# Kernel tuning notes

Measured on AMD Instinct MI355X. Metric: run time of the kernel, lower is better.

The kernel has to match this reference:

```python
import jax, jax.numpy as jnp
import numpy as np

N = 50000      # nodes
E = 1_000_000  # edges
EMB = 64       # out_channels per head
H = 2          # heads
HC = H * EMB   # 128 = concat output dim
HID = 128      # fc hidden size
NEG_SLOPE = 0.2


def _p(k, shape):
    return jax.random.normal(k, shape, dtype=jnp.float32) * 0.1


def setup_inputs() -> dict:
    key = jax.random.key(0)
    ks = jax.random.split(key, 24)
    inp = {
        "x": jax.random.normal(ks[0], (N, 1), dtype=jnp.float32),
        "edge_index": jax.random.randint(ks[1], (2, E), 0, N, dtype=jnp.int32),
        "edge_attr": jax.random.normal(ks[2], (E, 1), dtype=jnp.float32),
        "target_node_idx": 123,
        # conv1: GATv2Conv(1 -> 64, heads=2, edge_dim=1)
        "Wl1": _p(ks[3], (1, HC)), "bl1": jnp.zeros((HC,), jnp.float32),
        "Wr1": _p(ks[4], (1, HC)), "br1": jnp.zeros((HC,), jnp.float32),
        "We1": _p(ks[5], (1, HC)),
        "att1": _p(ks[6], (H, EMB)),
        "b1": jnp.zeros((HC,), jnp.float32),
        # conv2: GATv2Conv(128 -> 64, heads=2, edge_dim=1)
        "Wl2": _p(ks[7], (HC, HC)), "bl2": jnp.zeros((HC,), jnp.float32),
        "Wr2": _p(ks[8], (HC, HC)), "br2": jnp.zeros((HC,), jnp.float32),
        "We2": _p(ks[9], (1, HC)),
        "att2": _p(ks[10], (H, EMB)),
        "b2": jnp.zeros((HC,), jnp.float32),
        # fc: Linear(128 -> 128)
        "Wfc": _p(ks[11], (HC, HID)), "bfc": jnp.zeros((HID,), jnp.float32),
    }
    return inp


def add_self_loops(src, dst, edge_attr, n):
    loop = jnp.arange(n, dtype=src.dtype)
    fill = jnp.mean(edge_attr, axis=0)  # PyG fill_value='mean'
    src2 = jnp.concatenate([src, loop])
    dst2 = jnp.concatenate([dst, loop])
    ea2 = jnp.concatenate([edge_attr, jnp.broadcast_to(fill, (n, edge_attr.shape[1]))])
    return src2, dst2, ea2


def gatv2(x, src, dst, edge_attr, Wl, bl, Wr, br, We, att, bias, n):
    # x: [n, F_in]; per-head transforms -> [n, H, EMB]
    xl = (x @ Wl + bl).reshape(n, H, EMB)   # source transform
    xr = (x @ Wr + br).reshape(n, H, EMB)   # target transform
    ef = (edge_attr @ We).reshape(-1, H, EMB)
    # GATv2 attention: a^T LeakyReLU(xl_j + xr_i + e_ij)
    z = jax.nn.leaky_relu(xl[src] + xr[dst] + ef, NEG_SLOPE)  # [E', H, EMB]
    logits = jnp.einsum('ehc,hc->eh', z, att)                 # [E', H]
    # segment softmax over incoming edges per destination node
    m = jax.ops.segment_max(logits, dst, num_segments=n)[dst]
    ex = jnp.exp(logits - m)
    s = jax.ops.segment_sum(ex, dst, num_segments=n)[dst]
    alpha = ex / s                                            # [E', H]
    msg = xl[src] * alpha[:, :, None]                         # [E', H, EMB]
    out = jax.ops.segment_sum(msg, dst, num_segments=n)       # [n, H, EMB]
    return out.reshape(n, HC) + bias


def reference(x, edge_index, edge_attr, target_node_idx,
              Wl1, bl1, Wr1, br1, We1, att1, b1,
              Wl2, bl2, Wr2, br2, We2, att2, b2,
              Wfc, bfc):
    n = x.shape[0]
    src, dst, ea = add_self_loops(edge_index[0], edge_index[1], edge_attr, n)
    h = gatv2(x, src, dst, ea, Wl1, bl1, Wr1, br1, We1, att1, b1, n)
    h = jax.nn.relu(h)
    h = gatv2(h, src, dst, ea, Wl2, bl2, Wr2, br2, We2, att2, b2, n)
    target_emb = h[target_node_idx]          # [HC]
    return target_emb @ Wfc + bfc            # [HID]
```

## Files before the change

### kernel.cpp

```cpp
#include <hip/hip_runtime.h>
#include <hip/hip_bf16.h>

#define NEG_SLOPE 0.2f
#define THR    256
#define NB1    512
#define NB2    512
#define B1CAP  16
#define B2CAP  32
#define CAP1   512
#define CAPS   64
#define MAXDEG 256
#define NTAIL  (CAPS + 1)

#define OFF_PARTS  8
#define OFF_B1CNT  (OFF_PARTS + NB1)
#define OFF_B1SRC  (OFF_B1CNT + NB1)
#define OFF_B1EA   (OFF_B1SRC + NB1 * B1CAP)
#define OFF_B2CNT  (OFF_B1EA + NB1 * B1CAP)
#define OFF_B2SRC  (OFF_B2CNT + NB2)
#define OFF_B2DST  (OFF_B2SRC + NB2 * B2CAP)
#define OFF_B2EA   (OFF_B2DST + NB2 * B2CAP)
#define OFF_L1SRC  (OFF_B2EA + NB2 * B2CAP)
#define OFF_L1EA   (OFF_L1SRC + CAP1)
#define OFF_SLIST  (OFF_L1EA + CAP1)
#define OFF_XL2    (OFF_SLIST + CAPS)
#define OFF_XR2    (OFF_XL2 + CAPS * 128)

__device__ __forceinline__ float us2f(unsigned short s) {
    union { unsigned int u; float f; } c;
    c.u = ((unsigned int)s) << 16;
    return c.f;
}
template<bool F32>
__device__ __forceinline__ float tld(const void* p, int i) {
    if (F32) return ((const float*)p)[i];
    return us2f(((const unsigned short*)p)[i]);
}
__device__ __forceinline__ float ald_f(const float* p) {
    return __hip_atomic_load(p, __ATOMIC_RELAXED, __HIP_MEMORY_SCOPE_AGENT);
}

template<bool F32>
__device__ void scan1_body(const int* __restrict__ src, const int* __restrict__ dst,
                           const void* __restrict__ ea, int t, int E,
                           int* __restrict__ W) {
    __shared__ float sRed[4];
    __shared__ int   sCnt;
    __shared__ int   sIb[B1CAP];
    __shared__ float sFb[B1CAP];
    const int tid = threadIdx.x, bid = blockIdx.x;
    const int gid = bid * THR + tid, gs = NB1 * THR;
    const int E4 = E >> 2, rem = E & 3;
    float* parts = (float*)(W + OFF_PARTS);
    int*   b1cnt = W + OFF_B1CNT;
    int*   b1src = W + OFF_B1SRC;
    float* b1ea  = (float*)(W + OFF_B1EA);

    if (tid == 0) sCnt = 0;
    __syncthreads();
    float sum = 0.f;
    for (int j = gid; j < E4; j += gs) {
        int4 d4 = ((const int4*)dst)[j];
        float v0, v1, v2, v3;
        if (F32) {
            float4 e4 = ((const float4*)ea)[j];
            v0 = e4.x; v1 = e4.y; v2 = e4.z; v3 = e4.w;
        } else {
            ushort4 u4 = ((const ushort4*)ea)[j];
            v0 = us2f(u4.x); v1 = us2f(u4.y); v2 = us2f(u4.z); v3 = us2f(u4.w);
        }
        sum += (v0 + v1) + (v2 + v3);
        int base = 4 * j;
        if (d4.x == t) { int p = atomicAdd(&sCnt, 1); if (p < B1CAP) { sIb[p] = src[base+0]; sFb[p] = v0; } }
        if (d4.y == t) { int p = atomicAdd(&sCnt, 1); if (p < B1CAP) { sIb[p] = src[base+1]; sFb[p] = v1; } }
        if (d4.z == t) { int p = atomicAdd(&sCnt, 1); if (p < B1CAP) { sIb[p] = src[base+2]; sFb[p] = v2; } }
        if (d4.w == t) { int p = atomicAdd(&sCnt, 1); if (p < B1CAP) { sIb[p] = src[base+3]; sFb[p] = v3; } }
    }
    if (gid < rem) {
        int i = E4 * 4 + gid;
        float v = tld<F32>(ea, i);
        sum += v;
        if (dst[i] == t) { int p = atomicAdd(&sCnt, 1); if (p < B1CAP) { sIb[p] = src[i]; sFb[p] = v; } }
    }
    for (int o = 32; o > 0; o >>= 1) sum += __shfl_down(sum, o);
    if ((tid & 63) == 0) sRed[tid >> 6] = sum;
    __syncthreads();
    if (tid == 0) parts[bid] = sRed[0] + sRed[1] + sRed[2] + sRed[3];
    int bc = sCnt < B1CAP ? sCnt : B1CAP;
    if (tid == 0) b1cnt[bid] = bc;
    if (tid < bc) { b1src[bid * B1CAP + tid] = sIb[tid]; b1ea[bid * B1CAP + tid] = sFb[tid]; }
}

__global__ void __launch_bounds__(THR)
k_scan1(const void* __restrict__ x, const int* __restrict__ src,
        const int* __restrict__ dst, const void* __restrict__ ea,
        const int* __restrict__ tgt, int E, int* __restrict__ W) {
    __shared__ int sWeird;
    if (threadIdx.x == 0) sWeird = 0;
    __syncthreads();
    {
        const unsigned short* u = (const unsigned short*)x;
        int c = 0;
        for (int i = threadIdx.x; i < 2048; i += THR) {
            int e2 = (u[i] >> 7) & 0xFF;
            if (e2 == 0 || e2 >= 0xC0) c++;
        }
        for (int o = 32; o > 0; o >>= 1) c += __shfl_down(c, o);
        if ((threadIdx.x & 63) == 0) atomicAdd(&sWeird, c);
    }
    __syncthreads();
    bool f32 = sWeird >= 64;
    if (blockIdx.x == 0 && threadIdx.x == 0) W[3] = f32 ? 1 : 0;
    int t = tgt[0];
    if (f32) scan1_body<true >(src, dst, ea, t, E, W);
    else     scan1_body<false>(src, dst, ea, t, E, W);
}

template<bool F32>
__device__ void scan2_body(const int* __restrict__ src, const int* __restrict__ dst,
                           const void* __restrict__ ea, int tgt0, int E,
                           int* __restrict__ W) {
    __shared__ int   sS[CAPS];
    __shared__ int   sNs, sCnt;
    __shared__ int   sIb[B2CAP], sIb2[B2CAP];
    __shared__ float sFb[B2CAP];
    __shared__ int   sPfx[THR];
    __shared__ float sRed[4];
    const int tid = threadIdx.x, bid = blockIdx.x;
    const int gid = bid * THR + tid, gs = NB2 * THR;
    const int E4 = E >> 2, rem = E & 3;
    float* parts = (float*)(W + OFF_PARTS);
    int*   b1cnt = W + OFF_B1CNT;
    int*   b1src = W + OFF_B1SRC;
    float* b1ea  = (float*)(W + OFF_B1EA);
    int*   b2cnt = W + OFF_B2CNT;
    int*   b2src = W + OFF_B2SRC;
    int*   b2dst = W + OFF_B2DST;
    float* b2ea  = (float*)(W + OFF_B2EA);
    int*   l1src = W + OFF_L1SRC;
    float* l1ea  = (float*)(W + OFF_L1EA);
    int*   slist = W + OFF_SLIST;

    if (tid == 0) { sS[0] = tgt0; sNs = 1; sCnt = 0; }
    __syncthreads();
    for (int bk = tid; bk < NB1; bk += THR) {
        int c = b1cnt[bk]; if (c > B1CAP) c = B1CAP;
        for (int j = 0; j < c; j++) {
            int p = atomicAdd(&sNs, 1);
            if (p < CAPS) sS[p] = b1src[bk * B1CAP + j];
        }
    }
    __syncthreads();
    int ns = sNs < CAPS ? sNs : CAPS;

    #define CHECK(dv, idx)                                                     \
        do {                                                                   \
            for (int j_ = 0; j_ < ns; j_++) {                                  \
                if (sS[j_] == (dv)) {                                          \
                    int p_ = atomicAdd(&sCnt, 1);                              \
                    if (p_ < B2CAP) {                                          \
                        sIb[p_] = src[idx]; sIb2[p_] = (dv);                   \
                        sFb[p_] = tld<F32>(ea, idx);                           \
                    }                                                          \
                    break;                                                     \
                }                                                              \
            }                                                                  \
        } while (0)
    for (int j = gid; j < E4; j += gs) {
        int4 d4 = ((const int4*)dst)[j];
        int base = 4 * j;
        CHECK(d4.x, base + 0);
        CHECK(d4.y, base + 1);
        CHECK(d4.z, base + 2);
        CHECK(d4.w, base + 3);
    }
    if (gid < rem) { int i = E4 * 4 + gid; CHECK(dst[i], i); }
    #undef CHECK
    __syncthreads();
    int bc = sCnt < B2CAP ? sCnt : B2CAP;
    if (tid == 0) b2cnt[bid] = bc;
    if (tid < bc) {
        b2src[bid * B2CAP + tid] = sIb[tid];
        b2dst[bid * B2CAP + tid] = sIb2[tid];
        b2ea [bid * B2CAP + tid] = sFb[tid];
    }

    if (bid == 0) {
        __syncthreads();
        int c0  = b1cnt[2*tid];    if (c0  > B1CAP) c0  = B1CAP;
        int c1b = b1cnt[2*tid+1];  if (c1b > B1CAP) c1b = B1CAP;
        int c = c0 + c1b;
        sPfx[tid] = c;
        __syncthreads();
        for (int o = 1; o < THR; o <<= 1) {
            int v = (tid >= o) ? sPfx[tid - o] : 0;
            __syncthreads();
            sPfx[tid] += v;
            __syncthreads();
        }
        int base = sPfx[tid] - c;
        int c1tot = sPfx[THR - 1];
        for (int j = 0; j < c0; j++) {
            int p = base + j;
            if (p < CAP1 - 1) { l1src[p] = b1src[2*tid*B1CAP + j]; l1ea[p] = b1ea[2*tid*B1CAP + j]; }
        }
        for (int j = 0; j < c1b; j++) {
            int p = base + c0 + j;
            if (p < CAP1 - 1) { l1src[p] = b1src[(2*tid+1)*B1CAP + j]; l1ea[p] = b1ea[(2*tid+1)*B1CAP + j]; }
        }
        float s = parts[tid] + parts[tid + THR];
        for (int o = 32; o > 0; o >>= 1) s += __shfl_down(s, o);
        if ((tid & 63) == 0) sRed[tid >> 6] = s;
        __syncthreads();
        if (tid == 0) {
            float mean = (sRed[0] + sRed[1] + sRed[2] + sRed[3]) / (float)E;
            int c1 = c1tot < CAP1 - 1 ? c1tot : CAP1 - 1;
            l1src[c1] = tgt0; l1ea[c1] = mean;
            c1++;
            int nsl = 0;
            for (int e = 0; e < c1; e++) {
                int sv = l1src[e];
                bool f = false;
                for (int j = 0; j < nsl; j++) if (sS[j] == sv) { f = true; break; }
                if (!f && nsl < CAPS) { sS[nsl] = sv; nsl++; }
            }
            for (int j = 0; j < nsl; j++) slist[j] = sS[j];
            W[0] = c1; W[1] = nsl; W[4] = 0;
            ((float*)W)[5] = mean;
        }
    }
}

__global__ void __launch_bounds__(THR)
k_scan2(const int* __restrict__ src, const int* __restrict__ dst,
        const void* __restrict__ ea, const int* __restrict__ tgt,
        int E, int* __restrict__ W) {
    int t = tgt[0];
    if (W[3]) scan2_body<true >(src, dst, ea, t, E, W);
    else      scan2_body<false>(src, dst, ea, t, E, W);
}

template<bool F32>
__device__ void tail_body(
    const void* __restrict__ x, int tgt0,
    const void* Wl1, const void* bl1, const void* Wr1, const void* br1,
    const void* We1, const void* att1, const void* b1,
    const void* Wl2, const void* bl2, const void* Wr2, const void* br2,
    const void* We2, const void* att2, const void* b2v,
    const void* Wfc, const void* bfc,
    void* __restrict__ out, int* __restrict__ W)
{
    const int tid = threadIdx.x, bid = blockIdx.x;
    int*   b2cnt = W + OFF_B2CNT;
    int*   b2src = W + OFF_B2SRC;
    int*   b2dst = W + OFF_B2DST;
    float* b2ea  = (float*)(W + OFF_B2EA);
    int*   l1src = W + OFF_L1SRC;
    float* l1ea  = (float*)(W + OFF_L1EA);
    int*   slist = W + OFF_SLIST;
    float* xl2   = (float*)(W + OFF_XL2);
    float* xr2   = (float*)(W + OFF_XR2);

    int ns = W[1]; if (ns > CAPS) ns = CAPS;
    int c1 = W[0]; if (c1 > CAP1) c1 = CAP1;
    float mean = ((float*)W)[5];

    if (bid < ns) {
        __shared__ float sWl[128], sBl[128], sWe[128], sAtt[128], sB1[128], sBase[128];
        __shared__ float sXs[MAXDEG], sEa2[MAXDEG], sL0[MAXDEG], sL1[MAXDEG], sH[128];
        __shared__ int sCnt;
        int s = slist[bid];
        if (tid < 128) {
            sWl[tid] = tld<F32>(Wl1, tid);  sBl[tid] = tld<F32>(bl1, tid);
            sWe[tid] = tld<F32>(We1, tid);  sAtt[tid] = tld<F32>(att1, tid);
            sB1[tid] = tld<F32>(b1, tid);
            float xt = tld<F32>(x, s);
            sBase[tid] = xt * tld<F32>(Wr1, tid) + tld<F32>(br1, tid);
        }
        if (tid == 0) { sCnt = 1; sXs[0] = tld<F32>(x, s); sEa2[0] = mean; }
        __syncthreads();
        for (int bk = tid; bk < NB2; bk += THR) {
            int c = b2cnt[bk]; if (c > B2CAP) c = B2CAP;
            for (int j = 0; j < c; j++) {
                if (b2dst[bk * B2CAP + j] == s) {
                    int p = atomicAdd(&sCnt, 1);
                    if (p < MAXDEG) {
                        sXs[p] = tld<F32>(x, b2src[bk * B2CAP + j]);
                        sEa2[p] = b2ea[bk * B2CAP + j];
                    }
                }
            }
        }
        __syncthreads();
        int deg = sCnt < MAXDEG ? sCnt : MAXDEG;
        for (int i = tid; i < deg; i += THR) {
            float xs = sXs[i], eav = sEa2[i];
            float l0 = 0.f, l1v = 0.f;
            #pragma unroll 8
            for (int c2 = 0; c2 < 128; c2++) {
                float v = xs * sWl[c2] + sBl[c2] + sBase[c2] + eav * sWe[c2];
                v = v > 0.f ? v : NEG_SLOPE * v;
                float w = v * sAtt[c2];
                if (c2 < 64) l0 += w; else l1v += w;
            }
            sL0[i] = l0; sL1[i] = l1v;
        }
        __syncthreads();
        if (tid == 0) {
            float m0 = -1e30f, m1 = -1e30f;
            for (int i = 0; i < deg; i++) { m0 = fmaxf(m0, sL0[i]); m1 = fmaxf(m1, sL1[i]); }
            float s0 = 0.f, s1 = 0.f;
            for (int i = 0; i < deg; i++) {
                sL0[i] = __expf(sL0[i] - m0); s0 += sL0[i];
                sL1[i] = __expf(sL1[i] - m1); s1 += sL1[i];
            }
            float r0 = 1.f / s0, r1 = 1.f / s1;
            for (int i = 0; i < deg; i++) { sL0[i] *= r0; sL1[i] *= r1; }
        }
        __syncthreads();
        if (tid < 128) {
            bool hi = tid >= 64;
            float acc = 0.f;
            for (int i = 0; i < deg; i++) {
                float a = hi ? sL1[i] : sL0[i];
                acc += a * (sXs[i] * sWl[tid] + sBl[tid]);
            }
            acc += sB1[tid];
            sH[tid] = fmaxf(acc, 0.f);
        }
        __syncthreads();
        if (tid < 128) {
            float acc = tld<F32>(bl2, tid);
            #pragma unroll 16
            for (int k = 0; k < 128; k++) acc += sH[k] * tld<F32>(Wl2, k * 128 + tid);
            xl2[bid * 128 + tid] = acc;
            if (s == tgt0) {
                float a2 = tld<F32>(br2, tid);
                #pragma unroll 16
                for (int k = 0; k < 128; k++) a2 += sH[k] * tld<F32>(Wr2, k * 128 + tid);
                xr2[tid] = a2;
            }
        }
        __syncthreads();
        __threadfence();
        if (tid == 0)
            __hip_atomic_fetch_add(&W[4], 1, __ATOMIC_RELEASE, __HIP_MEMORY_SCOPE_AGENT);
    } else if (bid == CAPS) {
        __shared__ float sl0[CAP1], sl1[CAP1];
        __shared__ int sslot[CAP1];
        __shared__ float semb[128];
        __shared__ int sS[CAPS];
        if (tid == 0) {
            while (__hip_atomic_load(&W[4], __ATOMIC_RELAXED, __HIP_MEMORY_SCOPE_AGENT) < ns)
                __builtin_amdgcn_s_sleep(32);
        }
        __syncthreads();
        __threadfence();
        if (tid < ns) sS[tid] = slist[tid];
        __syncthreads();
        for (int e = tid; e < c1; e += THR) {
            int sv = l1src[e];
            int slot = 0;
            for (int j = 0; j < ns; j++) if (sS[j] == sv) { slot = j; break; }
            sslot[e] = slot;
        }
        __syncthreads();
        float xr = 0.f, we = 0.f, at = 0.f;
        if (tid < 128) { xr = ald_f(&xr2[tid]); we = tld<F32>(We2, tid); at = tld<F32>(att2, tid); }
        for (int e = 0; e < c1; e++) {
            float w = 0.f;
            if (tid < 128) {
                float v = ald_f(&xl2[sslot[e] * 128 + tid]) + xr + l1ea[e] * we;
                v = v > 0.f ? v : NEG_SLOPE * v;
                w = v * at;
            }
            for (int o = 32; o > 0; o >>= 1) w += __shfl_down(w, o);
            if (tid == 0)  sl0[e] = w;
            if (tid == 64) sl1[e] = w;
        }
        __syncthreads();
        if (tid == 0) {
            float m0 = -1e30f, m1 = -1e30f;
            for (int e = 0; e < c1; e++) { m0 = fmaxf(m0, sl0[e]); m1 = fmaxf(m1, sl1[e]); }
            float s0 = 0.f, s1 = 0.f;
            for (int e = 0; e < c1; e++) {
                sl0[e] = __expf(sl0[e] - m0); s0 += sl0[e];
                sl1[e] = __expf(sl1[e] - m1); s1 += sl1[e];
            }
            float r0 = 1.f / s0, r1 = 1.f / s1;
            for (int e = 0; e < c1; e++) { sl0[e] *= r0; sl1[e] *= r1; }
        }
        __syncthreads();
        if (tid < 128) {
            bool hi = tid >= 64;
            float acc = tld<F32>(b2v, tid);
            for (int e = 0; e < c1; e++) {
                float a = hi ? sl1[e] : sl0[e];
                acc += a * ald_f(&xl2[sslot[e] * 128 + tid]);
            }
            semb[tid] = acc;
        }
        __syncthreads();
        if (tid < 128) {
            float o = tld<F32>(bfc, tid);
            #pragma unroll 16
            for (int c2 = 0; c2 < 128; c2++) o += semb[c2] * tld<F32>(Wfc, c2 * 128 + tid);
            if (F32) ((float*)out)[tid] = o;
            else     ((__hip_bfloat16*)out)[tid] = __float2bfloat16(o);
        }
    }
}

__global__ void __launch_bounds__(THR)
k_tail(const void* x, const int* tgt,
       const void* Wl1, const void* bl1, const void* Wr1, const void* br1,
       const void* We1, const void* att1, const void* b1,
       const void* Wl2, const void* bl2, const void* Wr2, const void* br2,
       const void* We2, const void* att2, const void* b2v,
       const void* Wfc, const void* bfc,
       void* out, int* W)
{
    int t = tgt[0];
    if (W[3]) tail_body<true >(x, t, Wl1, bl1, Wr1, br1, We1, att1, b1,
                               Wl2, bl2, Wr2, br2, We2, att2, b2v, Wfc, bfc, out, W);
    else      tail_body<false>(x, t, Wl1, bl1, Wr1, br1, We1, att1, b1,
                               Wl2, bl2, Wr2, br2, We2, att2, b2v, Wfc, bfc, out, W);
}

extern "C" void kernel_launch(void* const* d_in, const int* in_sizes, int n_in,
                              void* d_out, int out_size, void* d_ws, size_t ws_size,
                              hipStream_t stream) {
    const void* x    = d_in[0];
    const int*  eidx = (const int*)d_in[1];
    const void* eattr= d_in[2];
    const int*  tgt  = (const int*)d_in[3];
    const void* Wl1 = d_in[4],  *bl1 = d_in[5],  *Wr1 = d_in[6],  *br1 = d_in[7];
    const void* We1 = d_in[8],  *att1= d_in[9],  *b1  = d_in[10];
    const void* Wl2 = d_in[11], *bl2 = d_in[12], *Wr2 = d_in[13], *br2 = d_in[14];
    const void* We2 = d_in[15], *att2= d_in[16], *b2v = d_in[17];
    const void* Wfc = d_in[18], *bfc = d_in[19];

    int E = in_sizes[1] / 2;
    const int* src = eidx;
    const int* dst = eidx + E;
    int* W = (int*)d_ws;

    k_scan1<<<NB1, THR, 0, stream>>>(x, src, dst, eattr, tgt, E, W);
    k_scan2<<<NB2, THR, 0, stream>>>(src, dst, eattr, tgt, E, W);
    k_tail <<<NTAIL, THR, 0, stream>>>(x, tgt, Wl1, bl1, Wr1, br1, We1, att1, b1,
                                       Wl2, bl2, Wr2, br2, We2, att2, b2v,
                                       Wfc, bfc, d_out, W);
}
```

Measured before the change: 155.9 us.

## Fuse second edge scan and tail into one kernel with per-block online softmax partials

Merges the second edge scan and the tail kernel into a single launch. Each scan block computes layer-1 attention logits for the matching edges it finds and keeps per-destination online-softmax partials (max, sum, weighted x). Block 0 waits on a global counter, merges all partials, builds layer-2 features for the 2-hop nodes, and finishes the target embedding and FC layer. This removes one kernel launch and the separate per-node gather pass over the bucket lists. In exchange, block 0 spin-waits for all 512 blocks and then runs the whole tail serially on one block, and correctness now depends on every block being resident or finishing.

```diff
diff --git a/kernel.cpp b/kernel.cpp
--- a/kernel.cpp
+++ b/kernel.cpp
@@ -6,25 +6,17 @@
 #define NB1    512
 #define NB2    512
 #define B1CAP  16
-#define B2CAP  32
+#define MCAP   32
 #define CAP1   512
 #define CAPS   64
-#define MAXDEG 256
-#define NTAIL  (CAPS + 1)
 
 #define OFF_PARTS  8
 #define OFF_B1CNT  (OFF_PARTS + NB1)
 #define OFF_B1SRC  (OFF_B1CNT + NB1)
 #define OFF_B1EA   (OFF_B1SRC + NB1 * B1CAP)
-#define OFF_B2CNT  (OFF_B1EA + NB1 * B1CAP)
-#define OFF_B2SRC  (OFF_B2CNT + NB2)
-#define OFF_B2DST  (OFF_B2SRC + NB2 * B2CAP)
-#define OFF_B2EA   (OFF_B2DST + NB2 * B2CAP)
-#define OFF_L1SRC  (OFF_B2EA + NB2 * B2CAP)
-#define OFF_L1EA   (OFF_L1SRC + CAP1)
-#define OFF_SLIST  (OFF_L1EA + CAP1)
-#define OFF_XL2    (OFF_SLIST + CAPS)
-#define OFF_XR2    (OFF_XL2 + CAPS * 128)
+#define OFF_TOUCH  (OFF_B1EA + NB1 * B1CAP)
+#define OFF_P2     (OFF_TOUCH + NB2 * 2)
+#define OFF_XL2    (OFF_P2 + NB2 * CAPS * 6)
 
 __device__ __forceinline__ float us2f(unsigned short s) {
     union { unsigned int u; float f; } c;
@@ -110,22 +102,23 @@
     }
     __syncthreads();
     bool f32 = sWeird >= 64;
-    if (blockIdx.x == 0 && threadIdx.x == 0) W[3] = f32 ? 1 : 0;
+    if (blockIdx.x == 0 && threadIdx.x == 0) { W[3] = f32 ? 1 : 0; W[4] = 0; }
     int t = tgt[0];
     if (f32) scan1_body<true >(src, dst, ea, t, E, W);
     else     scan1_body<false>(src, dst, ea, t, E, W);
 }
 
 template<bool F32>
-__device__ void scan2_body(const int* __restrict__ src, const int* __restrict__ dst,
-                           const void* __restrict__ ea, int tgt0, int E,
-                           int* __restrict__ W) {
-    __shared__ int   sS[CAPS];
-    __shared__ int   sNs, sCnt;
-    __shared__ int   sIb[B2CAP], sIb2[B2CAP];
-    __shared__ float sFb[B2CAP];
-    __shared__ int   sPfx[THR];
-    __shared__ float sRed[4];
+__device__ void rest_body(
+    const void* __restrict__ x, const int* __restrict__ src,
+    const int* __restrict__ dst, const void* __restrict__ ea, int tgt0, int E,
+    const void* Wl1, const void* bl1, const void* Wr1, const void* br1,
+    const void* We1, const void* att1, const void* b1c,
+    const void* Wl2, const void* bl2, const void* Wr2, const void* br2,
+    const void* We2, const void* att2, const void* b2v,
+    const void* Wfc, const void* bfc,
+    void* __restrict__ out, int* __restrict__ W)
+{
     const int tid = threadIdx.x, bid = blockIdx.x;
     const int gid = bid * THR + tid, gs = NB2 * THR;
     const int E4 = E >> 2, rem = E & 3;
@@ -133,34 +126,52 @@
     int*   b1cnt = W + OFF_B1CNT;
     int*   b1src = W + OFF_B1SRC;
     float* b1ea  = (float*)(W + OFF_B1EA);
-    int*   b2cnt = W + OFF_B2CNT;
-    int*   b2src = W + OFF_B2SRC;
-    int*   b2dst = W + OFF_B2DST;
-    float* b2ea  = (float*)(W + OFF_B2EA);
-    int*   l1src = W + OFF_L1SRC;
-    float* l1ea  = (float*)(W + OFF_L1EA);
-    int*   slist = W + OFF_SLIST;
-
-    if (tid == 0) { sS[0] = tgt0; sNs = 1; sCnt = 0; }
-    __syncthreads();
-    for (int bk = tid; bk < NB1; bk += THR) {
-        int c = b1cnt[bk]; if (c > B1CAP) c = B1CAP;
-        for (int j = 0; j < c; j++) {
-            int p = atomicAdd(&sNs, 1);
-            if (p < CAPS) sS[p] = b1src[bk * B1CAP + j];
-        }
-    }
-    __syncthreads();
-    int ns = sNs < CAPS ? sNs : CAPS;
+    unsigned long long* touched = (unsigned long long*)(W + OFF_TOUCH);
+    float* p2    = (float*)(W + OFF_P2);
+    float* xl2g  = (float*)(W + OFF_XL2);
+
+    __shared__ int   sS[CAPS];
+    __shared__ int   sPfx[THR];
+    __shared__ float sWl[128], sBl[128], sWr[128], sBr[128], sWe[128], sAtt[128];
+    __shared__ int   mSlot[MCAP], mSrc[MCAP];
+    __shared__ float mEa[MCAP], sL0[MCAP], sL1[MCAP];
+    __shared__ float pm0[CAPS], pz0[CAPS], pa0[CAPS], pm1[CAPS], pz1[CAPS], pa1[CAPS];
+    __shared__ int   sCnt, sNs;
+    __shared__ unsigned long long sMaskL;
+
+    {
+        int c0  = b1cnt[2*tid];   if (c0  > B1CAP) c0  = B1CAP;
+        int c1b = b1cnt[2*tid+1]; if (c1b > B1CAP) c1b = B1CAP;
+        int c = c0 + c1b;
+        sPfx[tid] = c;
+        __syncthreads();
+        for (int o = 1; o < THR; o <<= 1) {
+            int v = (tid >= o) ? sPfx[tid - o] : 0;
+            __syncthreads();
+            sPfx[tid] += v;
+            __syncthreads();
+        }
+        int base = sPfx[tid] - c;
+        for (int j = 0; j < c0; j++)  { int p = base + j;       if (p < CAPS-1) sS[p] = b1src[2*tid*B1CAP + j]; }
+        for (int j = 0; j < c1b; j++) { int p = base + c0 + j;  if (p < CAPS-1) sS[p] = b1src[(2*tid+1)*B1CAP + j]; }
+        __syncthreads();
+        if (tid == 0) {
+            int tot = sPfx[THR-1];
+            int nsb = tot < CAPS-1 ? tot : CAPS-1;
+            sS[nsb] = tgt0; sNs = nsb + 1; sCnt = 0;
+        }
+        __syncthreads();
+    }
+    int ns = sNs;
 
     #define CHECK(dv, idx)                                                     \
         do {                                                                   \
             for (int j_ = 0; j_ < ns; j_++) {                                  \
                 if (sS[j_] == (dv)) {                                          \
                     int p_ = atomicAdd(&sCnt, 1);                              \
-                    if (p_ < B2CAP) {                                          \
-                        sIb[p_] = src[idx]; sIb2[p_] = (dv);                   \
-                        sFb[p_] = tld<F32>(ea, idx);                           \
+                    if (p_ < MCAP) {                                           \
+                        mSlot[p_] = j_; mSrc[p_] = src[idx];                   \
+                        mEa[p_] = tld<F32>(ea, idx);                           \
                     }                                                          \
                     break;                                                     \
                 }                                                              \
@@ -177,18 +188,155 @@
     if (gid < rem) { int i = E4 * 4 + gid; CHECK(dst[i], i); }
     #undef CHECK
     __syncthreads();
-    int bc = sCnt < B2CAP ? sCnt : B2CAP;
-    if (tid == 0) b2cnt[bid] = bc;
-    if (tid < bc) {
-        b2src[bid * B2CAP + tid] = sIb[tid];
-        b2dst[bid * B2CAP + tid] = sIb2[tid];
-        b2ea [bid * B2CAP + tid] = sFb[tid];
-    }
-
-    if (bid == 0) {
-        __syncthreads();
-        int c0  = b1cnt[2*tid];    if (c0  > B1CAP) c0  = B1CAP;
-        int c1b = b1cnt[2*tid+1];  if (c1b > B1CAP) c1b = B1CAP;
+    int mcnt = sCnt < MCAP ? sCnt : MCAP;
+
+    if ((mcnt > 0 || bid == 0) && tid < 128) {
+        sWl[tid] = tld<F32>(Wl1, tid);  sBl[tid] = tld<F32>(bl1, tid);
+        sWr[tid] = tld<F32>(Wr1, tid);  sBr[tid] = tld<F32>(br1, tid);
+        sWe[tid] = tld<F32>(We1, tid);  sAtt[tid] = tld<F32>(att1, tid);
+    }
+    __syncthreads();
+
+    if (tid < 128) {
+        for (int e = 0; e < mcnt; e++) {
+            float xs = tld<F32>(x, mSrc[e]);
+            float xt = tld<F32>(x, sS[mSlot[e]]);
+            float ev = mEa[e];
+            float z = xs * sWl[tid] + sBl[tid] + xt * sWr[tid] + sBr[tid] + ev * sWe[tid];
+            z = z > 0.f ? z : NEG_SLOPE * z;
+            float w = z * sAtt[tid];
+            for (int o = 32; o > 0; o >>= 1) w += __shfl_down(w, o);
+            if (tid == 0)  sL0[e] = w;
+            if (tid == 64) sL1[e] = w;
+        }
+    }
+    __syncthreads();
+
+    if (tid == 0) {
+        unsigned long long mask = 0ull;
+        for (int e = 0; e < mcnt; e++) {
+            int s = mSlot[e];
+            float xs = tld<F32>(x, mSrc[e]);
+            float l0 = sL0[e], l1 = sL1[e];
+            if (!((mask >> s) & 1ull)) {
+                mask |= 1ull << s;
+                pm0[s] = l0; pz0[s] = 1.f; pa0[s] = xs;
+                pm1[s] = l1; pz1[s] = 1.f; pa1[s] = xs;
+            } else {
+                if (l0 <= pm0[s]) { float f = __expf(l0 - pm0[s]); pz0[s] += f; pa0[s] += f * xs; }
+                else { float f = __expf(pm0[s] - l0); pz0[s] = pz0[s]*f + 1.f; pa0[s] = pa0[s]*f + xs; pm0[s] = l0; }
+                if (l1 <= pm1[s]) { float f = __expf(l1 - pm1[s]); pz1[s] += f; pa1[s] += f * xs; }
+                else { float f = __expf(pm1[s] - l1); pz1[s] = pz1[s]*f + 1.f; pa1[s] = pa1[s]*f + xs; pm1[s] = l1; }
+            }
+        }
+        sMaskL = mask;
+    }
+    __syncthreads();
+
+    {
+        unsigned long long mask = sMaskL;
+        if (tid < CAPS && ((mask >> tid) & 1ull)) {
+            int base = ((bid << 6) + tid) * 6;
+            p2[base+0] = pm0[tid]; p2[base+1] = pz0[tid]; p2[base+2] = pa0[tid];
+            p2[base+3] = pm1[tid]; p2[base+4] = pz1[tid]; p2[base+5] = pa1[tid];
+        }
+        if (tid == 0) touched[bid] = mask;
+        __syncthreads();
+        __threadfence();
+        if (tid == 0)
+            __hip_atomic_fetch_add(&W[4], 1, __ATOMIC_RELEASE, __HIP_MEMORY_SCOPE_AGENT);
+    }
+    if (bid != 0) return;
+
+    if (tid == 0) {
+        while (__hip_atomic_load(&W[4], __ATOMIC_RELAXED, __HIP_MEMORY_SCOPE_AGENT) < NB2)
+            __builtin_amdgcn_s_sleep(16);
+        (void)__hip_atomic_load(&W[4], __ATOMIC_ACQUIRE, __HIP_MEMORY_SCOPE_AGENT);
+    }
+    __syncthreads();
+    __threadfence();
+
+    __shared__ float sRed[4];
+    __shared__ float sMean;
+    {
+        float s = parts[tid] + parts[tid + THR];
+        for (int o = 32; o > 0; o >>= 1) s += __shfl_down(s, o);
+        if ((tid & 63) == 0) sRed[tid >> 6] = s;
+        __syncthreads();
+        if (tid == 0) sMean = (sRed[0] + sRed[1] + sRed[2] + sRed[3]) / (float)E;
+        __syncthreads();
+    }
+    float mean = sMean;
+
+    __shared__ unsigned long long sMask[NB2];
+    for (int i = tid; i < NB2; i += THR)
+        sMask[i] = __hip_atomic_load(&touched[i], __ATOMIC_RELAXED, __HIP_MEMORY_SCOPE_AGENT);
+    __syncthreads();
+
+    __shared__ float sT0[CAPS], sT1[CAPS];
+    if (tid < ns) {
+        int node = sS[tid];
+        float xv = tld<F32>(x, node);
+        float l0 = 0.f, l1 = 0.f;
+        for (int c = 0; c < 128; c++) {
+            float z = xv * sWl[c] + sBl[c] + xv * sWr[c] + sBr[c] + mean * sWe[c];
+            z = z > 0.f ? z : NEG_SLOPE * z;
+            float w = z * sAtt[c];
+            if (c < 64) l0 += w; else l1 += w;
+        }
+        float M0 = l0, Z0 = 1.f, A0 = xv, M1 = l1, Z1 = 1.f, A1 = xv;
+        for (int bk = 0; bk < NB2; bk++) {
+            if ((sMask[bk] >> tid) & 1ull) {
+                int base = ((bk << 6) + tid) * 6;
+                float m0 = ald_f(&p2[base+0]), z0 = ald_f(&p2[base+1]), a0 = ald_f(&p2[base+2]);
+                float m1 = ald_f(&p2[base+3]), z1 = ald_f(&p2[base+4]), a1 = ald_f(&p2[base+5]);
+                if (m0 <= M0) { float f = __expf(m0 - M0); Z0 += z0 * f; A0 += a0 * f; }
+                else { float f = __expf(M0 - m0); Z0 = Z0*f + z0; A0 = A0*f + a0; M0 = m0; }
+                if (m1 <= M1) { float f = __expf(m1 - M1); Z1 += z1 * f; A1 += a1 * f; }
+                else { float f = __expf(M1 - m1); Z1 = Z1*f + z1; A1 = A1*f + a1; M1 = m1; }
+            }
+        }
+        sT0[tid] = A0 / Z0; sT1[tid] = A1 / Z1;
+    }
+    __syncthreads();
+
+    __shared__ float sH1[CAPS * 128];
+    __shared__ float sB1c[128];
+    if (tid < 128) sB1c[tid] = tld<F32>(b1c, tid);
+    __syncthreads();
+    for (int idx = tid; idx < ns * 128; idx += THR) {
+        int s = idx >> 7, c = idx & 127;
+        float T = (c < 64) ? sT0[s] : sT1[s];
+        sH1[idx] = fmaxf(T * sWl[c] + sBl[c] + sB1c[c], 0.f);
+    }
+    __syncthreads();
+
+    for (int idx = tid; idx < ns * 128; idx += THR) {
+        int s = idx >> 7, c = idx & 127;
+        float acc = tld<F32>(bl2, c);
+        #pragma unroll 16
+        for (int k = 0; k < 128; k++) acc += sH1[(s << 7) + k] * tld<F32>(Wl2, k * 128 + c);
+        xl2g[idx] = acc;
+    }
+    __shared__ float sXr[128];
+    __shared__ int sTs;
+    if (tid == 0) { int ts = 0; for (int j = 0; j < ns; j++) if (sS[j] == tgt0) { ts = j; break; } sTs = ts; }
+    __syncthreads();
+    int ts = sTs;
+    if (tid < 128) {
+        float acc = tld<F32>(br2, tid);
+        #pragma unroll 16
+        for (int k = 0; k < 128; k++) acc += sH1[(ts << 7) + k] * tld<F32>(Wr2, k * 128 + tid);
+        sXr[tid] = acc;
+    }
+    __syncthreads();
+
+    __shared__ int   sL1src[CAP1];
+    __shared__ float sL1ea[CAP1];
+    __shared__ int   sC1;
+    {
+        int c0  = b1cnt[2*tid];   if (c0  > B1CAP) c0  = B1CAP;
+        int c1b = b1cnt[2*tid+1]; if (c1b > B1CAP) c1b = B1CAP;
         int c = c0 + c1b;
         sPfx[tid] = c;
         __syncthreads();
@@ -199,231 +347,87 @@
             __syncthreads();
         }
         int base = sPfx[tid] - c;
-        int c1tot = sPfx[THR - 1];
-        for (int j = 0; j < c0; j++) {
-            int p = base + j;
-            if (p < CAP1 - 1) { l1src[p] = b1src[2*tid*B1CAP + j]; l1ea[p] = b1ea[2*tid*B1CAP + j]; }
-        }
-        for (int j = 0; j < c1b; j++) {
-            int p = base + c0 + j;
-            if (p < CAP1 - 1) { l1src[p] = b1src[(2*tid+1)*B1CAP + j]; l1ea[p] = b1ea[(2*tid+1)*B1CAP + j]; }
-        }
-        float s = parts[tid] + parts[tid + THR];
-        for (int o = 32; o > 0; o >>= 1) s += __shfl_down(s, o);
-        if ((tid & 63) == 0) sRed[tid >> 6] = s;
+        for (int j = 0; j < c0; j++)  { int p = base + j;      if (p < CAP1-1) { sL1src[p] = b1src[2*tid*B1CAP + j];     sL1ea[p] = b1ea[2*tid*B1CAP + j]; } }
+        for (int j = 0; j < c1b; j++) { int p = base + c0 + j; if (p < CAP1-1) { sL1src[p] = b1src[(2*tid+1)*B1CAP + j]; sL1ea[p] = b1ea[(2*tid+1)*B1CAP + j]; } }
         __syncthreads();
         if (tid == 0) {
-            float mean = (sRed[0] + sRed[1] + sRed[2] + sRed[3]) / (float)E;
-            int c1 = c1tot < CAP1 - 1 ? c1tot : CAP1 - 1;
-            l1src[c1] = tgt0; l1ea[c1] = mean;
-            c1++;
-            int nsl = 0;
-            for (int e = 0; e < c1; e++) {
-                int sv = l1src[e];
-                bool f = false;
-                for (int j = 0; j < nsl; j++) if (sS[j] == sv) { f = true; break; }
-                if (!f && nsl < CAPS) { sS[nsl] = sv; nsl++; }
-            }
-            for (int j = 0; j < nsl; j++) slist[j] = sS[j];
-            W[0] = c1; W[1] = nsl; W[4] = 0;
-            ((float*)W)[5] = mean;
-        }
+            int t2 = sPfx[THR-1]; if (t2 > CAP1-1) t2 = CAP1-1;
+            sL1src[t2] = tgt0; sL1ea[t2] = mean; sC1 = t2 + 1;
+        }
+        __syncthreads();
+    }
+    int c1 = sC1;
+
+    __shared__ int sslot[CAP1];
+    for (int e = tid; e < c1; e += THR) {
+        int sv = sL1src[e]; int slot = 0;
+        for (int j = 0; j < ns; j++) if (sS[j] == sv) { slot = j; break; }
+        sslot[e] = slot;
+    }
+    __syncthreads();
+
+    __shared__ float sl0[CAP1], sl1[CAP1];
+    float xr = 0.f, we2 = 0.f, at2 = 0.f;
+    if (tid < 128) { xr = sXr[tid]; we2 = tld<F32>(We2, tid); at2 = tld<F32>(att2, tid); }
+    for (int e = 0; e < c1; e++) {
+        float w = 0.f;
+        if (tid < 128) {
+            float v = xl2g[(sslot[e] << 7) + tid] + xr + sL1ea[e] * we2;
+            v = v > 0.f ? v : NEG_SLOPE * v;
+            w = v * at2;
+        }
+        for (int o = 32; o > 0; o >>= 1) w += __shfl_down(w, o);
+        if (tid == 0)  sl0[e] = w;
+        if (tid == 64) sl1[e] = w;
+    }
+    __syncthreads();
+    if (tid == 0) {
+        float m0 = -1e30f, m1 = -1e30f;
+        for (int e = 0; e < c1; e++) { m0 = fmaxf(m0, sl0[e]); m1 = fmaxf(m1, sl1[e]); }
+        float s0 = 0.f, s1 = 0.f;
+        for (int e = 0; e < c1; e++) {
+            sl0[e] = __expf(sl0[e] - m0); s0 += sl0[e];
+            sl1[e] = __expf(sl1[e] - m1); s1 += sl1[e];
+        }
+        float r0 = 1.f / s0, r1 = 1.f / s1;
+        for (int e = 0; e < c1; e++) { sl0[e] *= r0; sl1[e] *= r1; }
+    }
+    __syncthreads();
+
+    __shared__ float semb[128];
+    if (tid < 128) {
+        bool hi = tid >= 64;
+        float acc = tld<F32>(b2v, tid);
+        for (int e = 0; e < c1; e++) {
+            float a = hi ? sl1[e] : sl0[e];
+            acc += a * xl2g[(sslot[e] << 7) + tid];
+        }
+        semb[tid] = acc;
+    }
+    __syncthreads();
+    if (tid < 128) {
+        float o = tld<F32>(bfc, tid);
+        #pragma unroll 16
+        for (int c = 0; c < 128; c++) o += semb[c] * tld<F32>(Wfc, c * 128 + tid);
+        if (F32) ((float*)out)[tid] = o;
+        else     ((__hip_bfloat16*)out)[tid] = __float2bfloat16(o);
     }
 }
 
 __global__ void __launch_bounds__(THR)
-k_scan2(const int* __restrict__ src, const int* __restrict__ dst,
-        const void* __restrict__ ea, const int* __restrict__ tgt,
-        int E, int* __restrict__ W) {
-    int t = tgt[0];
-    if (W[3]) scan2_body<true >(src, dst, ea, t, E, W);
-    else      scan2_body<false>(src, dst, ea, t, E, W);
-}
-
-template<bool F32>
-__device__ void tail_body(
-    const void* __restrict__ x, int tgt0,
-    const void* Wl1, const void* bl1, const void* Wr1, const void* br1,
-    const void* We1, const void* att1, const void* b1,
-    const void* Wl2, const void* bl2, const void* Wr2, const void* br2,
-    const void* We2, const void* att2, const void* b2v,
-    const void* Wfc, const void* bfc,
-    void* __restrict__ out, int* __restrict__ W)
-{
-    const int tid = threadIdx.x, bid = blockIdx.x;
-    int*   b2cnt = W + OFF_B2CNT;
-    int*   b2src = W + OFF_B2SRC;
-    int*   b2dst = W + OFF_B2DST;
-    float* b2ea  = (float*)(W + OFF_B2EA);
-    int*   l1src = W + OFF_L1SRC;
-    float* l1ea  = (float*)(W + OFF_L1EA);
-    int*   slist = W + OFF_SLIST;
-    float* xl2   = (float*)(W + OFF_XL2);
-    float* xr2   = (float*)(W + OFF_XR2);
-
-    int ns = W[1]; if (ns > CAPS) ns = CAPS;
-    int c1 = W[0]; if (c1 > CAP1) c1 = CAP1;
-    float mean = ((float*)W)[5];
-
-    if (bid < ns) {
-        __shared__ float sWl[128], sBl[128], sWe[128], sAtt[128], sB1[128], sBase[128];
-        __shared__ float sXs[MAXDEG], sEa2[MAXDEG], sL0[MAXDEG], sL1[MAXDEG], sH[128];
-        __shared__ int sCnt;
-        int s = slist[bid];
-        if (tid < 128) {
-            sWl[tid] = tld<F32>(Wl1, tid);  sBl[tid] = tld<F32>(bl1, tid);
-            sWe[tid] = tld<F32>(We1, tid);  sAtt[tid] = tld<F32>(att1, tid);
-            sB1[tid] = tld<F32>(b1, tid);
-            float xt = tld<F32>(x, s);
-            sBase[tid] = xt * tld<F32>(Wr1, tid) + tld<F32>(br1, tid);
-        }
-        if (tid == 0) { sCnt = 1; sXs[0] = tld<F32>(x, s); sEa2[0] = mean; }
-        __syncthreads();
-        for (int bk = tid; bk < NB2; bk += THR) {
-            int c = b2cnt[bk]; if (c > B2CAP) c = B2CAP;
-            for (int j = 0; j < c; j++) {
-                if (b2dst[bk * B2CAP + j] == s) {
-                    int p = atomicAdd(&sCnt, 1);
-                    if (p < MAXDEG) {
-                        sXs[p] = tld<F32>(x, b2src[bk * B2CAP + j]);
-                        sEa2[p] = b2ea[bk * B2CAP + j];
-                    }
-                }
-            }
-        }
-        __syncthreads();
-        int deg = sCnt < MAXDEG ? sCnt : MAXDEG;
-        for (int i = tid; i < deg; i += THR) {
-            float xs = sXs[i], eav = sEa2[i];
-            float l0 = 0.f, l1v = 0.f;
-            #pragma unroll 8
-            for (int c2 = 0; c2 < 128; c2++) {
-                float v = xs * sWl[c2] + sBl[c2] + sBase[c2] + eav * sWe[c2];
-                v = v > 0.f ? v : NEG_SLOPE * v;
-                float w = v * sAtt[c2];
-                if (c2 < 64) l0 += w; else l1v += w;
-            }
-            sL0[i] = l0; sL1[i] = l1v;
-        }
-        __syncthreads();
-        if (tid == 0) {
-            float m0 = -1e30f, m1 = -1e30f;
-            for (int i = 0; i < deg; i++) { m0 = fmaxf(m0, sL0[i]); m1 = fmaxf(m1, sL1[i]); }
-            float s0 = 0.f, s1 = 0.f;
-            for (int i = 0; i < deg; i++) {
-                sL0[i] = __expf(sL0[i] - m0); s0 += sL0[i];
-                sL1[i] = __expf(sL1[i] - m1); s1 += sL1[i];
-            }
-            float r0 = 1.f / s0, r1 = 1.f / s1;
-            for (int i = 0; i < deg; i++) { sL0[i] *= r0; sL1[i] *= r1; }
-        }
-        __syncthreads();
-        if (tid < 128) {
-            bool hi = tid >= 64;
-            float acc = 0.f;
-            for (int i = 0; i < deg; i++) {
-                float a = hi ? sL1[i] : sL0[i];
-                acc += a * (sXs[i] * sWl[tid] + sBl[tid]);
-            }
-            acc += sB1[tid];
-            sH[tid] = fmaxf(acc, 0.f);
-        }
-        __syncthreads();
-        if (tid < 128) {
-            float acc = tld<F32>(bl2, tid);
-            #pragma unroll 16
-            for (int k = 0; k < 128; k++) acc += sH[k] * tld<F32>(Wl2, k * 128 + tid);
-            xl2[bid * 128 + tid] = acc;
-            if (s == tgt0) {
-                float a2 = tld<F32>(br2, tid);
-                #pragma unroll 16
-                for (int k = 0; k < 128; k++) a2 += sH[k] * tld<F32>(Wr2, k * 128 + tid);
-                xr2[tid] = a2;
-            }
-        }
-        __syncthreads();
-        __threadfence();
-        if (tid == 0)
-            __hip_atomic_fetch_add(&W[4], 1, __ATOMIC_RELEASE, __HIP_MEMORY_SCOPE_AGENT);
-    } else if (bid == CAPS) {
-        __shared__ float sl0[CAP1], sl1[CAP1];
-        __shared__ int sslot[CAP1];
-        __shared__ float semb[128];
-        __shared__ int sS[CAPS];
-        if (tid == 0) {
-            while (__hip_atomic_load(&W[4], __ATOMIC_RELAXED, __HIP_MEMORY_SCOPE_AGENT) < ns)
-                __builtin_amdgcn_s_sleep(32);
-        }
-        __syncthreads();
-        __threadfence();
-        if (tid < ns) sS[tid] = slist[tid];
-        __syncthreads();
-        for (int e = tid; e < c1; e += THR) {
-            int sv = l1src[e];
-            int slot = 0;
-            for (int j = 0; j < ns; j++) if (sS[j] == sv) { slot = j; break; }
-            sslot[e] = slot;
-        }
-        __syncthreads();
-        float xr = 0.f, we = 0.f, at = 0.f;
-        if (tid < 128) { xr = ald_f(&xr2[tid]); we = tld<F32>(We2, tid); at = tld<F32>(att2, tid); }
-        for (int e = 0; e < c1; e++) {
-            float w = 0.f;
-            if (tid < 128) {
-                float v = ald_f(&xl2[sslot[e] * 128 + tid]) + xr + l1ea[e] * we;
-                v = v > 0.f ? v : NEG_SLOPE * v;
-                w = v * at;
-            }
-            for (int o = 32; o > 0; o >>= 1) w += __shfl_down(w, o);
-            if (tid == 0)  sl0[e] = w;
-            if (tid == 64) sl1[e] = w;
-        }
-        __syncthreads();
-        if (tid == 0) {
-            float m0 = -1e30f, m1 = -1e30f;
-            for (int e = 0; e < c1; e++) { m0 = fmaxf(m0, sl0[e]); m1 = fmaxf(m1, sl1[e]); }
-            float s0 = 0.f, s1 = 0.f;
-            for (int e = 0; e < c1; e++) {
-                sl0[e] = __expf(sl0[e] - m0); s0 += sl0[e];
-                sl1[e] = __expf(sl1[e] - m1); s1 += sl1[e];
-            }
-            float r0 = 1.f / s0, r1 = 1.f / s1;
-            for (int e = 0; e < c1; e++) { sl0[e] *= r0; sl1[e] *= r1; }
-        }
-        __syncthreads();
-        if (tid < 128) {
-            bool hi = tid >= 64;
-            float acc = tld<F32>(b2v, tid);
-            for (int e = 0; e < c1; e++) {
-                float a = hi ? sl1[e] : sl0[e];
-                acc += a * ald_f(&xl2[sslot[e] * 128 + tid]);
-            }
-            semb[tid] = acc;
-        }
-        __syncthreads();
-        if (tid < 128) {
-            float o = tld<F32>(bfc, tid);
-            #pragma unroll 16
-            for (int c2 = 0; c2 < 128; c2++) o += semb[c2] * tld<F32>(Wfc, c2 * 128 + tid);
-            if (F32) ((float*)out)[tid] = o;
-            else     ((__hip_bfloat16*)out)[tid] = __float2bfloat16(o);
-        }
-    }
-}
-
-__global__ void __launch_bounds__(THR)
-k_tail(const void* x, const int* tgt,
+k_rest(const void* x, const int* src, const int* dst, const void* ea,
+       const int* tgt, int E,
        const void* Wl1, const void* bl1, const void* Wr1, const void* br1,
-       const void* We1, const void* att1, const void* b1,
+       const void* We1, const void* att1, const void* b1c,
        const void* Wl2, const void* bl2, const void* Wr2, const void* br2,
        const void* We2, const void* att2, const void* b2v,
        const void* Wfc, const void* bfc,
        void* out, int* W)
 {
     int t = tgt[0];
-    if (W[3]) tail_body<true >(x, t, Wl1, bl1, Wr1, br1, We1, att1, b1,
+    if (W[3]) rest_body<true >(x, src, dst, ea, t, E, Wl1, bl1, Wr1, br1, We1, att1, b1c,
                                Wl2, bl2, Wr2, br2, We2, att2, b2v, Wfc, bfc, out, W);
-    else      tail_body<false>(x, t, Wl1, bl1, Wr1, br1, We1, att1, b1,
+    else      rest_body<false>(x, src, dst, ea, t, E, Wl1, bl1, Wr1, br1, We1, att1, b1c,
                                Wl2, bl2, Wr2, br2, We2, att2, b2v, Wfc, bfc, out, W);
 }
 
@@ -446,8 +450,8 @@
     int* W = (int*)d_ws;
 
     k_scan1<<<NB1, THR, 0, stream>>>(x, src, dst, eattr, tgt, E, W);
-    k_scan2<<<NB2, THR, 0, stream>>>(src, dst, eattr, tgt, E, W);
-    k_tail <<<NTAIL, THR, 0, stream>>>(x, tgt, Wl1, bl1, Wr1, br1, We1, att1, b1,
-                                       Wl2, bl2, Wr2, br2, We2, att2, b2v,
-                                       Wfc, bfc, d_out, W);
-}
+    k_rest <<<NB2, THR, 0, stream>>>(x, src, dst, eattr, tgt, E,
+                                     Wl1, bl1, Wr1, br1, We1, att1, b1,
+                                     Wl2, bl2, Wr2, br2, We2, att2, b2v,
+                                     Wfc, bfc, d_out, W);
+}
```

After: 298.5 us. +91.5%, slower.
